# Kernel tuning notes

Hardware: AMD Instinct MI355X
Metric: run time of the kernel (lower is better)

Reference implementation:

```python
import jax, jax.numpy as jnp
import numpy as np

B, C, D, H, W = 4, 128, 16, 16, 16
INNER = 64  # channels // reduction


def setup_inputs() -> dict:
    key = jax.random.key(0)
    ks = jax.random.split(key, 4)
    s = 0.02
    return {
        "x": jax.random.normal(ks[0], (B, C, D, H, W), dtype=jnp.float32),
        "Wq": jax.random.normal(ks[1], (INNER, C), dtype=jnp.float32) * s,
        "bq": jnp.zeros((INNER,), dtype=jnp.float32),
        "Wk": jax.random.normal(ks[2], (INNER, C), dtype=jnp.float32) * s,
        "bk": jnp.zeros((INNER,), dtype=jnp.float32),
        "Wv": jax.random.normal(ks[3], (C, C), dtype=jnp.float32) * s,
        "bv": jnp.zeros((C,), dtype=jnp.float32),
        "gamma": jnp.zeros((1,), dtype=jnp.float32),
    }


def reference(x, Wq, bq, Wk, bk, Wv, bv, gamma):
    b, c, d, h, w = x.shape
    n = d * h * w
    inner = Wq.shape[0]
    scale = inner ** (-0.5)
    xf = x.reshape(b, c, n)  # flatten spatial dims
    # 1x1 Conv3d == per-position channel matmul
    q = jnp.einsum('oc,bcn->bon', Wq, xf) + bq[None, :, None]  # [B, inner, N]
    k = jnp.einsum('oc,bcn->bon', Wk, xf) + bk[None, :, None]  # [B, inner, N]
    v = jnp.einsum('oc,bcn->bon', Wv, xf) + bv[None, :, None]  # [B, C, N]
    # attn[b, n, m] = softmax_m(q[:, :, n] . k[:, :, m] * scale)
    attn = jax.nn.softmax(jnp.einsum('bon,bom->bnm', q, k) * scale, axis=-1)
    # out = v @ attn^T  -> out[b, c, n] = sum_m v[b, c, m] * attn[b, n, m]
    out = jnp.einsum('bcm,bnm->bcn', v, attn).reshape(b, c, d, h, w)
    return x + gamma[0] * out
```

## Files before the change

### kernel.cpp

```cpp
#include <hip/hip_runtime.h>
#include <cstdint>

#define B_ 4
#define C_ 128
#define INNER_ 64
#define N_ 4096
#define SPLITS 6
#define KT 64

typedef __attribute__((ext_vector_type(8))) short short8;
typedef __attribute__((ext_vector_type(4))) short bf16x4;
typedef __attribute__((ext_vector_type(4))) float f32x4;
typedef __attribute__((ext_vector_type(2))) unsigned u32x2;

typedef const __attribute__((address_space(1))) void* gp_t;
typedef __attribute__((address_space(3))) void* lp_t;

__device__ __forceinline__ short f2bf(float f) {
  unsigned u = __builtin_bit_cast(unsigned, f);
  unsigned r = (u + 0x7FFFu + ((u >> 16) & 1u)) >> 16;
  return (short)r;
}
__device__ __forceinline__ float bf2f(short s) {
  return __builtin_bit_cast(float, ((unsigned)(unsigned short)s) << 16);
}
__device__ __forceinline__ unsigned pk2(float lo, float hi) {
#if __has_builtin(__builtin_amdgcn_cvt_pk_bf16_f32)
  typedef __attribute__((ext_vector_type(2))) __bf16 bfp;
  bfp v = __builtin_amdgcn_cvt_pk_bf16_f32(lo, hi);
  return __builtin_bit_cast(unsigned, v);
#else
  return (unsigned)(unsigned short)f2bf(lo) | ((unsigned)(unsigned short)f2bf(hi) << 16);
#endif
}

__device__ __forceinline__ f32x4 mfma16(bf16x4 a, bf16x4 b, f32x4 c) {
#if __has_builtin(__builtin_amdgcn_mfma_f32_16x16x16bf16_1k)
  return __builtin_amdgcn_mfma_f32_16x16x16bf16_1k(a, b, c, 0, 0, 0);
#elif __has_builtin(__builtin_amdgcn_mfma_f32_16x16x16_bf16)
  return __builtin_amdgcn_mfma_f32_16x16x16_bf16(a, b, c, 0, 0, 0);
#else
  f32x4 d;
  asm volatile("v_mfma_f32_16x16x16_bf16 %0, %1, %2, %3"
               : "=v"(d) : "v"(a), "v"(b), "v"(c));
  return d;
#endif
}

__global__ __launch_bounds__(256) void pack_kernel(
    const float* __restrict__ Wq, const float* __restrict__ bq,
    const float* __restrict__ Wk, const float* __restrict__ bk,
    const float* __restrict__ Wv, const float* __restrict__ bv,
    short* __restrict__ wp, float* __restrict__ bp)
{
  const int idx = blockIdx.x * 256 + threadIdx.x;
  const int o = idx >> 7, c = idx & 127;
  float v;
  if (o < 64)       v = Wq[o * C_ + c];
  else if (o < 128) v = Wk[(o - 64) * C_ + c];
  else              v = Wv[(o - 128) * C_ + c];
  wp[idx] = f2bf(v);
  if (c == 0)
    bp[o] = (o < 64) ? bq[o] : (o < 128) ? bk[o - 64] : bv[o - 128];
}

__global__ __launch_bounds__(256) void qkv_kernel(
    const float* __restrict__ x, const short* __restrict__ wp,
    const float* __restrict__ bp,
    short* __restrict__ qg, short* __restrict__ kg, short* __restrict__ vg)
{
  __shared__ short xT[32 * 136];
  __shared__ short outb[256 * 40];
  __shared__ float biasL[256];

  const int tid = threadIdx.x;
  const int b   = blockIdx.x >> 7;
  const int n0  = (blockIdx.x & 127) << 5;

  biasL[tid] = bp[tid];
  const float* xb = x + (size_t)b * C_ * N_ + n0;
  for (int i = tid; i < 1024; i += 256) {
    const int c = i >> 3, seg = i & 7;
    const float4 v = *(const float4*)&xb[(size_t)c * N_ + seg * 4];
    xT[(seg * 4 + 0) * 136 + c] = f2bf(v.x);
    xT[(seg * 4 + 1) * 136 + c] = f2bf(v.y);
    xT[(seg * 4 + 2) * 136 + c] = f2bf(v.z);
    xT[(seg * 4 + 3) * 136 + c] = f2bf(v.w);
  }
  __syncthreads();

  const int w = tid >> 6, lane = tid & 63, quad = lane >> 4, l16 = lane & 15;

  short8 xf[2][4];
#pragma unroll
  for (int nt = 0; nt < 2; ++nt)
#pragma unroll
    for (int kk = 0; kk < 4; ++kk)
      xf[nt][kk] = *(const short8*)&xT[(nt * 16 + l16) * 136 + kk * 32 + quad * 8];

  if (w < 2) {
    const int obase = w * 64;
#pragma unroll
    for (int ot = 0; ot < 4; ++ot) {
      const int o = obase + ot * 16 + l16;
      short8 wf[4];
#pragma unroll
      for (int kk = 0; kk < 4; ++kk)
        wf[kk] = *(const short8*)&wp[(size_t)o * 128 + kk * 32 + quad * 8];
      const float bias = biasL[o];
#pragma unroll
      for (int nt = 0; nt < 2; ++nt) {
        f32x4 acc = (f32x4){0.f, 0.f, 0.f, 0.f};
#pragma unroll
        for (int kk = 0; kk < 4; ++kk)
          acc = __builtin_amdgcn_mfma_f32_16x16x32_bf16(xf[nt][kk], wf[kk], acc, 0, 0, 0);
#pragma unroll
        for (int r = 0; r < 4; ++r)
          outb[o * 40 + nt * 16 + quad * 4 + r] = f2bf(acc[r] + bias);
      }
    }
  } else {
    const int ob2 = (w - 2) * 64;
#pragma unroll
    for (int ot = 0; ot < 4; ++ot) {
      const int orow = 128 + ob2 + ot * 16 + l16;
      short8 wf[4];
#pragma unroll
      for (int kk = 0; kk < 4; ++kk)
        wf[kk] = *(const short8*)&wp[(size_t)orow * 128 + kk * 32 + quad * 8];
#pragma unroll
      for (int nt = 0; nt < 2; ++nt) {
        f32x4 acc = (f32x4){0.f, 0.f, 0.f, 0.f};
#pragma unroll
        for (int kk = 0; kk < 4; ++kk)
          acc = __builtin_amdgcn_mfma_f32_16x16x32_bf16(wf[kk], xf[nt][kk], acc, 0, 0, 0);
#pragma unroll
        for (int r = 0; r < 4; ++r) {
          const int o_r = 128 + ob2 + ot * 16 + quad * 4 + r;
          outb[o_r * 40 + nt * 16 + l16] = f2bf(acc[r] + biasL[o_r]);
        }
      }
    }
  }
  __syncthreads();

  {
    const int n = tid >> 3, oc = tid & 7;
    short8 qv, kv;
#pragma unroll
    for (int j = 0; j < 8; ++j) {
      qv[j] = outb[(oc * 8 + j) * 40 + n];
      kv[j] = outb[(64 + oc * 8 + j) * 40 + n];
    }
    *(short8*)&qg[(((size_t)b * N_ + n0 + n) << 6) + oc * 8] = qv;
    *(short8*)&kg[(((size_t)b * N_ + n0 + n) << 6) + oc * 8] = kv;
  }
  {
    const int T = n0 >> 6;
    const int k4base = (n0 & 63) >> 2;
#pragma unroll
    for (int rep = 0; rep < 2; ++rep) {
      const int idx2 = rep * 256 + tid;
      const int c0  = idx2 & 63;
      const int k4l = idx2 >> 6;
      const bf16x4 lo = *(const bf16x4*)&outb[(128 + 2 * c0) * 40 + k4l * 4];
      const bf16x4 hi = *(const bf16x4*)&outb[(128 + 2 * c0 + 1) * 40 + k4l * 4];
      short8 vv;
#pragma unroll
      for (int j = 0; j < 4; ++j) { vv[j] = lo[j]; vv[4 + j] = hi[j]; }
      const size_t tb = (((size_t)b * 64 + T) * 16 + k4base + k4l) * 512 + c0 * 8;
      *(short8*)&vg[tb] = vv;
    }
  }
}

__global__ __launch_bounds__(256, 3) void attn_kernel(
    const short* __restrict__ qb, const short* __restrict__ kb,
    const short* __restrict__ vb,
    short* __restrict__ Opart, float* __restrict__ lbuf)
{
  __shared__ short kbuf[2][4096];
  __shared__ short vbuf[2][8192];

  const int tid = threadIdx.x;
  const int bid = blockIdx.x;
  const int s   = bid % 6;
  const int qt  = (bid / 6) & 31;
  const int b   = bid / 192;
  const int m0  = qt << 7;
  const int w   = tid >> 6, lane = tid & 63, quad = lane >> 4, l16 = lane & 15;
  const int rbase = m0 + w * 32;

  const int t0  = (s * 64) / 6;
  const int NTs = ((s + 1) * 64) / 6 - t0;

  const float kS = 0.125f * 1.44269504088896340736f;

  short8 qa[2][2];
#pragma unroll
  for (int mt = 0; mt < 2; ++mt)
#pragma unroll
    for (int kk = 0; kk < 2; ++kk)
      qa[mt][kk] = *(const short8*)&qb[((size_t)b * N_ + rbase + mt * 16 + l16) * 64 + kk * 32 + quad * 8];

  float lsum[2] = {0.f, 0.f};
  f32x4 accO[8][2];
#pragma unroll
  for (int vt = 0; vt < 8; ++vt)
#pragma unroll
    for (int mt = 0; mt < 2; ++mt) accO[vt][mt] = (f32x4){0.f, 0.f, 0.f, 0.f};

  auto dma_tile = [&](int kt, int d) {
    const int T = t0 + kt;
    const short* kbp = kb + (((size_t)b * N_ + T * 64) << 6);
#pragma unroll
    for (int t = 0; t < 2; ++t) {
      const int p = (w * 2 + t) * 64 + lane;
      const int key = p >> 3, jm = (p & 7) ^ (key & 7);
      const short* src = kbp + (key << 6) + jm * 8;
      __builtin_amdgcn_global_load_lds((gp_t)src, (lp_t)&kbuf[d][(w * 2 + t) * 512], 16, 0, 0);
    }
    const short* vtp = vb + ((size_t)b * 64 + T) * 8192;
#pragma unroll
    for (int t = 0; t < 4; ++t) {
      const int p = (w * 4 + t) * 64 + lane;
      __builtin_amdgcn_global_load_lds((gp_t)(vtp + p * 8), (lp_t)&vbuf[d][(w * 4 + t) * 512], 16, 0, 0);
    }
  };

  dma_tile(0, 0);

  for (int kt = 0; kt < NTs; ++kt) {
    __syncthreads();
    if (kt + 1 < NTs) dma_tile(kt + 1, (kt + 1) & 1);
    const int d = kt & 1;

    bf16x4 pbf[4][2];
#pragma unroll
    for (int ct = 0; ct < 4; ++ct) {
      const short8 kf0 = *(const short8*)&kbuf[d][((ct * 16 + l16) << 6) + ((quad ^ (l16 & 7)) << 3)];
      const short8 kf1 = *(const short8*)&kbuf[d][((ct * 16 + l16) << 6) + (((4 + quad) ^ (l16 & 7)) << 3)];
#pragma unroll
      for (int mt = 0; mt < 2; ++mt) {
        f32x4 st = (f32x4){0.f, 0.f, 0.f, 0.f};
        st = __builtin_amdgcn_mfma_f32_16x16x32_bf16(kf0, qa[mt][0], st, 0, 0, 0);
        st = __builtin_amdgcn_mfma_f32_16x16x32_bf16(kf1, qa[mt][1], st, 0, 0, 0);
        const float p0 = exp2f(st[0] * kS);
        const float p1 = exp2f(st[1] * kS);
        const float p2 = exp2f(st[2] * kS);
        const float p3 = exp2f(st[3] * kS);
        lsum[mt] += (p0 + p1) + (p2 + p3);
        u32x2 pp;
        pp[0] = pk2(p0, p1);
        pp[1] = pk2(p2, p3);
        pbf[ct][mt] = __builtin_bit_cast(bf16x4, pp);
      }
    }

#pragma unroll
    for (int vt = 0; vt < 8; ++vt) {
#pragma unroll
      for (int ct = 0; ct < 4; ++ct) {
        const bf16x4 vf = *(const bf16x4*)&vbuf[d][(ct * 4 + quad) * 512 + (vt * 16 + l16) * 4];
        accO[vt][0] = mfma16(vf, pbf[ct][0], accO[vt][0]);
        accO[vt][1] = mfma16(vf, pbf[ct][1], accO[vt][1]);
      }
    }
  }

#pragma unroll
  for (int mt = 0; mt < 2; ++mt) {
    lsum[mt] += __shfl_xor(lsum[mt], 16);
    lsum[mt] += __shfl_xor(lsum[mt], 32);
  }
  if (quad == 0) {
#pragma unroll
    for (int mt = 0; mt < 2; ++mt)
      lbuf[((size_t)b * SPLITS + s) * N_ + rbase + mt * 16 + l16] = lsum[mt];
  }
#pragma unroll
  for (int vt = 0; vt < 8; ++vt) {
#pragma unroll
    for (int mt = 0; mt < 2; ++mt) {
#pragma unroll
      for (int r = 0; r < 4; ++r) {
        const int ch = vt * 16 + quad * 4 + r;
        Opart[(((size_t)b * SPLITS + s) * C_ + ch) * N_ + rbase + mt * 16 + l16] =
            f2bf(accO[vt][mt][r]);
      }
    }
  }
}

__global__ __launch_bounds__(256) void combine_kernel(
    const float* __restrict__ x, const float* __restrict__ gamma,
    const short* __restrict__ Opart, const float* __restrict__ lbuf,
    float* __restrict__ out)
{
  __shared__ float linvL[64];
  const int tid = threadIdx.x;
  const int b   = blockIdx.x >> 6;
  const int n0  = (blockIdx.x & 63) << 6;

  if (tid < 64) {
    float L = 0.f;
#pragma unroll
    for (int s = 0; s < SPLITS; ++s) L += lbuf[((size_t)b * SPLITS + s) * N_ + n0 + tid];
    linvL[tid] = 1.f / L;
  }
  __syncthreads();

  const float g = gamma[0];
  const int n4 = (tid & 15) * 4, cb = tid >> 4;
#pragma unroll
  for (int cp = 0; cp < 8; ++cp) {
    const int c = cp * 16 + cb;
    float acc[4] = {0.f, 0.f, 0.f, 0.f};
#pragma unroll
    for (int s = 0; s < SPLITS; ++s) {
      const bf16x4 o4 = *(const bf16x4*)&Opart[(((size_t)b * SPLITS + s) * C_ + c) * N_ + n0 + n4];
#pragma unroll
      for (int j = 0; j < 4; ++j) acc[j] += bf2f(o4[j]);
    }
    const size_t xi = ((size_t)b * C_ + c) * N_ + n0 + n4;
    const float4 xv = *(const float4*)&x[xi];
    float4 ov;
    ov.x = xv.x + g * acc[0] * linvL[n4 + 0];
    ov.y = xv.y + g * acc[1] * linvL[n4 + 1];
    ov.z = xv.z + g * acc[2] * linvL[n4 + 2];
    ov.w = xv.w + g * acc[3] * linvL[n4 + 3];
    *(float4*)&out[xi] = ov;
  }
}

extern "C" void kernel_launch(void* const* d_in, const int* in_sizes, int n_in,
                              void* d_out, int out_size, void* d_ws, size_t ws_size,
                              hipStream_t stream) {
  const float* x     = (const float*)d_in[0];
  const float* Wq    = (const float*)d_in[1];
  const float* bq    = (const float*)d_in[2];
  const float* Wk    = (const float*)d_in[3];
  const float* bk    = (const float*)d_in[4];
  const float* Wv    = (const float*)d_in[5];
  const float* bv    = (const float*)d_in[6];
  const float* gamma = (const float*)d_in[7];
  float* out = (float*)d_out;

  short* qb = (short*)d_ws;
  short* kb = qb + (size_t)B_ * N_ * INNER_;
  short* vb = kb + (size_t)B_ * N_ * INNER_;
  short* Opart = vb + (size_t)B_ * C_ * N_;
  float* lbuf  = (float*)(Opart + (size_t)B_ * SPLITS * C_ * N_);
  float* bp    = lbuf + (size_t)B_ * SPLITS * N_;
  short* wp    = (short*)(bp + 256);

  pack_kernel<<<128, 256, 0, stream>>>(Wq, bq, Wk, bk, Wv, bv, wp, bp);
  qkv_kernel<<<B_ * (N_ / 32), 256, 0, stream>>>(x, wp, bp, qb, kb, vb);
  attn_kernel<<<B_ * 32 * SPLITS, 256, 0, stream>>>(qb, kb, vb, Opart, lbuf);
  combine_kernel<<<B_ * (N_ / 64), 256, 0, stream>>>(x, gamma, Opart, lbuf, out);
}
```

Before: 134.0 us.

## Use 8 key splits with 32-key tiles, prescale Q, use raw exp2

```diff
diff --git a/kernel.cpp b/kernel.cpp
--- a/kernel.cpp
+++ b/kernel.cpp
@@ -5,8 +5,9 @@
 #define C_ 128
 #define INNER_ 64
 #define N_ 4096
-#define SPLITS 6
-#define KT 64
+#define SPLITS 8
+#define KT 32
+#define NTS 16
 
 typedef __attribute__((ext_vector_type(8))) short short8;
 typedef __attribute__((ext_vector_type(4))) short bf16x4;
@@ -23,6 +24,13 @@
 }
 __device__ __forceinline__ float bf2f(short s) {
   return __builtin_bit_cast(float, ((unsigned)(unsigned short)s) << 16);
+}
+__device__ __forceinline__ float fexp2(float x) {
+#if __has_builtin(__builtin_amdgcn_exp2f)
+  return __builtin_amdgcn_exp2f(x);
+#else
+  return exp2f(x);
+#endif
 }
 __device__ __forceinline__ unsigned pk2(float lo, float hi) {
 #if __has_builtin(__builtin_amdgcn_cvt_pk_bf16_f32)
@@ -76,6 +84,7 @@
   const int tid = threadIdx.x;
   const int b   = blockIdx.x >> 7;
   const int n0  = (blockIdx.x & 127) << 5;
+  const float QSC = 0.125f * 1.44269504088896340736f;
 
   biasL[tid] = bp[tid];
   const float* xb = x + (size_t)b * C_ * N_ + n0;
@@ -100,6 +109,7 @@
 
   if (w < 2) {
     const int obase = w * 64;
+    const float osc = (w == 0) ? QSC : 1.0f;
 #pragma unroll
     for (int ot = 0; ot < 4; ++ot) {
       const int o = obase + ot * 16 + l16;
@@ -116,7 +126,7 @@
           acc = __builtin_amdgcn_mfma_f32_16x16x32_bf16(xf[nt][kk], wf[kk], acc, 0, 0, 0);
 #pragma unroll
         for (int r = 0; r < 4; ++r)
-          outb[o * 40 + nt * 16 + quad * 4 + r] = f2bf(acc[r] + bias);
+          outb[o * 40 + nt * 16 + quad * 4 + r] = f2bf((acc[r] + bias) * osc);
       }
     }
   } else {
@@ -156,8 +166,7 @@
     *(short8*)&kg[(((size_t)b * N_ + n0 + n) << 6) + oc * 8] = kv;
   }
   {
-    const int T = n0 >> 6;
-    const int k4base = (n0 & 63) >> 2;
+    const int T = n0 >> 5;
 #pragma unroll
     for (int rep = 0; rep < 2; ++rep) {
       const int idx2 = rep * 256 + tid;
@@ -168,34 +177,29 @@
       short8 vv;
 #pragma unroll
       for (int j = 0; j < 4; ++j) { vv[j] = lo[j]; vv[4 + j] = hi[j]; }
-      const size_t tb = (((size_t)b * 64 + T) * 16 + k4base + k4l) * 512 + c0 * 8;
+      const size_t tb = (((size_t)b * 128 + T) * 8 + k4l) * 512 + c0 * 8;
       *(short8*)&vg[tb] = vv;
     }
   }
 }
 
-__global__ __launch_bounds__(256, 3) void attn_kernel(
+__global__ __launch_bounds__(256, 4) void attn_kernel(
     const short* __restrict__ qb, const short* __restrict__ kb,
     const short* __restrict__ vb,
     short* __restrict__ Opart, float* __restrict__ lbuf)
 {
-  __shared__ short kbuf[2][4096];
-  __shared__ short vbuf[2][8192];
+  __shared__ short kbuf[2][2048];
+  __shared__ short vbuf[2][4096];
 
   const int tid = threadIdx.x;
   const int bid = blockIdx.x;
-  const int s   = bid % 6;
-  const int qt  = (bid / 6) & 31;
-  const int b   = bid / 192;
+  const int s   = bid & 7;
+  const int qt  = (bid >> 3) & 31;
+  const int b   = bid >> 8;
   const int m0  = qt << 7;
   const int w   = tid >> 6, lane = tid & 63, quad = lane >> 4, l16 = lane & 15;
   const int rbase = m0 + w * 32;
 
-  const int t0  = (s * 64) / 6;
-  const int NTs = ((s + 1) * 64) / 6 - t0;
-
-  const float kS = 0.125f * 1.44269504088896340736f;
-
   short8 qa[2][2];
 #pragma unroll
   for (int mt = 0; mt < 2; ++mt)
@@ -211,33 +215,33 @@
     for (int mt = 0; mt < 2; ++mt) accO[vt][mt] = (f32x4){0.f, 0.f, 0.f, 0.f};
 
   auto dma_tile = [&](int kt, int d) {
-    const int T = t0 + kt;
-    const short* kbp = kb + (((size_t)b * N_ + T * 64) << 6);
+    const int T = s * NTS + kt;
+    const short* kbp = kb + (((size_t)b * N_ + T * 32) << 6);
+    {
+      const int p = w * 64 + lane;
+      const int key = p >> 3, jm = (p & 7) ^ (key & 7);
+      __builtin_amdgcn_global_load_lds((gp_t)(kbp + (key << 6) + jm * 8),
+                                       (lp_t)&kbuf[d][w * 512], 16, 0, 0);
+    }
+    const short* vtp = vb + ((size_t)b * 128 + T) * 4096;
 #pragma unroll
     for (int t = 0; t < 2; ++t) {
       const int p = (w * 2 + t) * 64 + lane;
-      const int key = p >> 3, jm = (p & 7) ^ (key & 7);
-      const short* src = kbp + (key << 6) + jm * 8;
-      __builtin_amdgcn_global_load_lds((gp_t)src, (lp_t)&kbuf[d][(w * 2 + t) * 512], 16, 0, 0);
-    }
-    const short* vtp = vb + ((size_t)b * 64 + T) * 8192;
-#pragma unroll
-    for (int t = 0; t < 4; ++t) {
-      const int p = (w * 4 + t) * 64 + lane;
-      __builtin_amdgcn_global_load_lds((gp_t)(vtp + p * 8), (lp_t)&vbuf[d][(w * 4 + t) * 512], 16, 0, 0);
+      __builtin_amdgcn_global_load_lds((gp_t)(vtp + p * 8),
+                                       (lp_t)&vbuf[d][(w * 2 + t) * 512], 16, 0, 0);
     }
   };
 
   dma_tile(0, 0);
 
-  for (int kt = 0; kt < NTs; ++kt) {
+  for (int kt = 0; kt < NTS; ++kt) {
     __syncthreads();
-    if (kt + 1 < NTs) dma_tile(kt + 1, (kt + 1) & 1);
+    if (kt + 1 < NTS) dma_tile(kt + 1, (kt + 1) & 1);
     const int d = kt & 1;
 
-    bf16x4 pbf[4][2];
-#pragma unroll
-    for (int ct = 0; ct < 4; ++ct) {
+    bf16x4 pbf[2][2];
+#pragma unroll
+    for (int ct = 0; ct < 2; ++ct) {
       const short8 kf0 = *(const short8*)&kbuf[d][((ct * 16 + l16) << 6) + ((quad ^ (l16 & 7)) << 3)];
       const short8 kf1 = *(const short8*)&kbuf[d][((ct * 16 + l16) << 6) + (((4 + quad) ^ (l16 & 7)) << 3)];
 #pragma unroll
@@ -245,10 +249,10 @@
         f32x4 st = (f32x4){0.f, 0.f, 0.f, 0.f};
         st = __builtin_amdgcn_mfma_f32_16x16x32_bf16(kf0, qa[mt][0], st, 0, 0, 0);
         st = __builtin_amdgcn_mfma_f32_16x16x32_bf16(kf1, qa[mt][1], st, 0, 0, 0);
-        const float p0 = exp2f(st[0] * kS);
-        const float p1 = exp2f(st[1] * kS);
-        const float p2 = exp2f(st[2] * kS);
-        const float p3 = exp2f(st[3] * kS);
+        const float p0 = fexp2(st[0]);
+        const float p1 = fexp2(st[1]);
+        const float p2 = fexp2(st[2]);
+        const float p3 = fexp2(st[3]);
         lsum[mt] += (p0 + p1) + (p2 + p3);
         u32x2 pp;
         pp[0] = pk2(p0, p1);
@@ -260,7 +264,7 @@
 #pragma unroll
     for (int vt = 0; vt < 8; ++vt) {
 #pragma unroll
-      for (int ct = 0; ct < 4; ++ct) {
+      for (int ct = 0; ct < 2; ++ct) {
         const bf16x4 vf = *(const bf16x4*)&vbuf[d][(ct * 4 + quad) * 512 + (vt * 16 + l16) * 4];
         accO[vt][0] = mfma16(vf, pbf[ct][0], accO[vt][0]);
         accO[vt][1] = mfma16(vf, pbf[ct][1], accO[vt][1]);
```

Measured after the change: 126.7 us. -5.4%, faster.
